# Kernel tuning notes

Measured on AMD Instinct MI355X. Metric: run time of the kernel, lower is better.

## Reference

```python
import jax, jax.numpy as jnp
import numpy as np

TOP_K = 2
CAPACITY_FACTOR = 1.25
EPSILON = 1e-06
AUX_LOSS_WEIGHT = 0.01
NUM_EXPERTS = 64


def setup_inputs() -> dict:
    key = jax.random.key(0)
    k1, k2 = jax.random.split(key, 2)
    x = jax.random.normal(k1, (32768, 1024), dtype=jnp.float32)
    w_gate = jax.random.normal(k2, (NUM_EXPERTS, 1024), dtype=jnp.float32) * 0.02
    b_gate = jnp.zeros((NUM_EXPERTS,), dtype=jnp.float32)
    return {"x": x, "w_gate": w_gate, "b_gate": b_gate}


def reference(x, w_gate, b_gate):
    # x: [N, dim]; w_gate: [E, dim]; b_gate: [E]
    n_tokens = x.shape[0]
    capacity = int(CAPACITY_FACTOR * n_tokens)  # static, like torch int(...)

    logits = jnp.einsum('nd,ed->ne', x, w_gate) + b_gate          # [N, E]
    raw_gate_scores = jax.nn.softmax(logits, axis=-1)             # [N, E]

    _, top_k_indices = jax.lax.top_k(raw_gate_scores, TOP_K)      # [N, k]
    rows = jnp.arange(n_tokens)[:, None]                          # [N, 1]
    mask = jnp.zeros_like(raw_gate_scores).at[rows, top_k_indices].set(1.0)

    masked_gate_scores = raw_gate_scores * mask                   # [N, E]
    denominators = masked_gate_scores.sum(axis=0, keepdims=True) + EPSILON
    gate_scores = masked_gate_scores / denominators * capacity    # [N, E]

    importance = raw_gate_scores.mean(axis=0)                     # [E]
    load = mask.mean(axis=0)                                      # [E]
    aux_loss = AUX_LOSS_WEIGHT * (importance * load).mean() * (NUM_EXPERTS ** 2)
    return gate_scores, aux_loss
```

## Files before the change

### kernel.cpp

```cpp
#include <hip/hip_runtime.h>
#include <cstdint>

typedef float f32x2 __attribute__((ext_vector_type(2)));
typedef float f32x4 __attribute__((ext_vector_type(4)));

constexpr int N_TOK = 32768;
constexpr int DIM   = 1024;
constexpr int NEXP  = 64;
constexpr float CAPACITY = 40960.0f;
constexpr float EPS_DEN  = 1e-6f;

__device__ float  g_sums[192];
__device__ float4 g_rec[N_TOK];

__global__ void init_sums() {
    if (threadIdx.x < 192) g_sums[threadIdx.x] = 0.0f;
}

__global__ __launch_bounds__(256, 2)
void gate_main(const float* __restrict__ x,
               const float* __restrict__ wg,
               const float* __restrict__ bg) {
    __shared__ float acT[NEXP * 4 * 64];
    __shared__ float ws[192];

    const int tid  = threadIdx.x;
    const int lane = tid & 63;
    const int q    = __builtin_amdgcn_readfirstlane(tid >> 6);
    const int row  = blockIdx.x * 64 + lane;

    if (tid < 192) ws[tid] = 0.0f;

    float acc[NEXP];
#pragma unroll
    for (int e = 0; e < NEXP; ++e) acc[e] = 0.0f;

    const float* xq = x  + (size_t)row * DIM + q * 256;
    const float* wq = wg + q * 256;

    f32x4 xa0, xa1, xa2, xa3;
    {
        const f32x4* xp = (const f32x4*)xq;
        xa0 = xp[0]; xa1 = xp[1]; xa2 = xp[2]; xa3 = xp[3];
    }

#pragma unroll 1
    for (int kc = 0; kc < 16; ++kc) {
        f32x4 xb0, xb1, xb2, xb3;
        if (kc + 1 < 16) {
            const f32x4* xp = (const f32x4*)(xq + (kc + 1) * 16);
            xb0 = xp[0]; xb1 = xp[1]; xb2 = xp[2]; xb3 = xp[3];
        }
#pragma unroll
        for (int e = 0; e < NEXP; ++e) {
            const f32x4* wp = (const f32x4*)(wq + e * DIM + kc * 16);
            f32x4 w0 = wp[0], w1 = wp[1], w2 = wp[2], w3 = wp[3];
            f32x2 t = {0.0f, 0.0f};
            t = __builtin_elementwise_fma((f32x2){xa0.x, xa0.y}, (f32x2){w0.x, w0.y}, t);
            t = __builtin_elementwise_fma((f32x2){xa0.z, xa0.w}, (f32x2){w0.z, w0.w}, t);
            t = __builtin_elementwise_fma((f32x2){xa1.x, xa1.y}, (f32x2){w1.x, w1.y}, t);
            t = __builtin_elementwise_fma((f32x2){xa1.z, xa1.w}, (f32x2){w1.z, w1.w}, t);
            t = __builtin_elementwise_fma((f32x2){xa2.x, xa2.y}, (f32x2){w2.x, w2.y}, t);
            t = __builtin_elementwise_fma((f32x2){xa2.z, xa2.w}, (f32x2){w2.z, w2.w}, t);
            t = __builtin_elementwise_fma((f32x2){xa3.x, xa3.y}, (f32x2){w3.x, w3.y}, t);
            t = __builtin_elementwise_fma((f32x2){xa3.z, xa3.w}, (f32x2){w3.z, w3.w}, t);
            acc[e] += t.x + t.y;
        }
        xa0 = xb0; xa1 = xb1; xa2 = xb2; xa3 = xb3;
    }

#pragma unroll
    for (int e = 0; e < NEXP; ++e)
        acT[(e * 4 + q) * 64 + lane] = acc[e];
    __syncthreads();

    if (q == 0) {
        float lg[NEXP];
#pragma unroll
        for (int e = 0; e < NEXP; ++e) {
            lg[e] = (acT[(e * 4 + 0) * 64 + lane] + acT[(e * 4 + 1) * 64 + lane])
                  + (acT[(e * 4 + 2) * 64 + lane] + acT[(e * 4 + 3) * 64 + lane]);
            lg[e] += bg[e];
        }

        float b1 = -INFINITY, b2 = -INFINITY; int i1 = 0, i2 = 0;
#pragma unroll
        for (int e = 0; e < NEXP; ++e) {
            float v = lg[e];
            if (v > b1)      { b2 = b1; i2 = i1; b1 = v; i1 = e; }
            else if (v > b2) { b2 = v;  i2 = e; }
        }

        float s = 0.0f;
#pragma unroll
        for (int e = 0; e < NEXP; ++e) {
            float t = expf(lg[e] - b1);
            lg[e] = t;
            s += t;
        }
        const float inv  = 1.0f / s;
        const float raw1 = inv;
        const float raw2 = expf(b2 - b1) * inv;

        float* rawT = acT;
#pragma unroll
        for (int e = 0; e < NEXP; ++e)
            rawT[lane * 65 + e] = lg[e] * inv;
        __asm__ volatile("" ::: "memory");
        float imp = 0.0f;
#pragma unroll
        for (int t = 0; t < 64; ++t)
            imp += rawT[t * 65 + lane];
        atomicAdd(&g_sums[64 + lane], imp);

        atomicAdd(&ws[i1], raw1);
        atomicAdd(&ws[i2], raw2);
        atomicAdd(&ws[128 + i1], 1.0f);
        atomicAdd(&ws[128 + i2], 1.0f);
        g_rec[row] = make_float4(raw1, raw2,
                                 __int_as_float(i1), __int_as_float(i2));
    }

    __syncthreads();
    if (tid < 64)                     atomicAdd(&g_sums[tid], ws[tid]);
    else if (tid >= 128 && tid < 192) atomicAdd(&g_sums[tid], ws[tid]);
}

__global__ __launch_bounds__(256)
void scatter_out(float* __restrict__ out) {
    __shared__ float scale_s[NEXP];
    int tid = threadIdx.x;
    if (tid < NEXP) {
        float den = g_sums[tid];
        scale_s[tid] = CAPACITY / (den + EPS_DEN);
        if (blockIdx.x == 0) {
            float prod = g_sums[64 + tid] * g_sums[128 + tid];
#pragma unroll
            for (int off = 32; off; off >>= 1) prod += __shfl_xor(prod, off);
            if (tid == 0) {
                out[(size_t)N_TOK * NEXP] =
                    0.64f * prod / ((float)N_TOK * (float)N_TOK);
            }
        }
    }
    __syncthreads();

    int row = blockIdx.x * 16 + (tid >> 4);
    int g   = tid & 15;

    float4 rec = g_rec[row];
    int i1 = __float_as_int(rec.z);
    int i2 = __float_as_int(rec.w);
    float s1 = rec.x * scale_s[i1];
    float s2 = rec.y * scale_s[i2];

    int base = g * 4;
    float4 o;
    o.x = (i1 == base + 0) ? s1 : ((i2 == base + 0) ? s2 : 0.0f);
    o.y = (i1 == base + 1) ? s1 : ((i2 == base + 1) ? s2 : 0.0f);
    o.z = (i1 == base + 2) ? s1 : ((i2 == base + 2) ? s2 : 0.0f);
    o.w = (i1 == base + 3) ? s1 : ((i2 == base + 3) ? s2 : 0.0f);

    ((float4*)out)[(size_t)row * 16 + g] = o;
}

extern "C" void kernel_launch(void* const* d_in, const int* in_sizes, int n_in,
                              void* d_out, int out_size, void* d_ws, size_t ws_size,
                              hipStream_t stream) {
    const float* x  = (const float*)d_in[0];
    const float* wg = (const float*)d_in[1];
    const float* bg = (const float*)d_in[2];
    float* out = (float*)d_out;

    hipLaunchKernelGGL(init_sums, dim3(1), dim3(256), 0, stream);
    hipLaunchKernelGGL(gate_main, dim3(N_TOK / 64), dim3(256), 0, stream,
                       x, wg, bg);
    hipLaunchKernelGGL(scatter_out, dim3(N_TOK / 16), dim3(256), 0, stream, out);
}
```

Before: 408.3 us.

## Split gating GEMM into register-tiled split-K kernel plus separate combine kernel

Replaces the per-row dot-product gate kernel with a split-K register-tiled GEMM. Each thread computes a 16-token by 4-expert tile, with weights staged through double-buffered, XOR-swizzled shared memory. Partial sums for the four K quarters go to a global buffer, and a new combine kernel does the bias, softmax, top-2 and statistics. This aims to remove the redundant per-thread weight loads and raise FMA reuse, at the cost of an extra 32 MB round trip for partials and one more launch.

Measured after the change: 578.0 us. +41.5%, slower.

```diff
diff --git a/kernel.cpp b/kernel.cpp
--- a/kernel.cpp
+++ b/kernel.cpp
@@ -1,7 +1,6 @@
 #include <hip/hip_runtime.h>
 #include <cstdint>
 
-typedef float f32x2 __attribute__((ext_vector_type(2)));
 typedef float f32x4 __attribute__((ext_vector_type(4)));
 
 constexpr int N_TOK = 32768;
@@ -12,118 +11,162 @@
 
 __device__ float  g_sums[192];
 __device__ float4 g_rec[N_TOK];
+__device__ float  g_part[4][NEXP][N_TOK];
 
 __global__ void init_sums() {
     if (threadIdx.x < 192) g_sums[threadIdx.x] = 0.0f;
 }
 
-__global__ __launch_bounds__(256, 2)
-void gate_main(const float* __restrict__ x,
-               const float* __restrict__ wg,
-               const float* __restrict__ bg) {
-    __shared__ float acT[NEXP * 4 * 64];
+#define MT 16
+#define NT 4
+
+__global__ __launch_bounds__(512, 2)
+void gemm_part(const float* __restrict__ x, const float* __restrict__ wg) {
+    __shared__ f32x4 wbuf[2][NEXP * 16];
+
+    const int tid  = threadIdx.x;
+    const int cc   = tid & 15;
+    const int rs   = tid >> 4;
+    const int kq   = blockIdx.x & 3;
+    const int tg   = blockIdx.x >> 2;
+    const int tbase = tg * 512 + rs * MT;
+
+    const float* xrow = x + (size_t)tbase * DIM + kq * 256;
+    const float* wq   = wg + kq * 256;
+
+    float acc[MT][NT];
+#pragma unroll
+    for (int m = 0; m < MT; ++m)
+#pragma unroll
+        for (int n = 0; n < NT; ++n) acc[m][n] = 0.0f;
+
+    f32x4 xa[MT], xb[MT], wst[2];
+
+#define PF(X, kk) do { _Pragma("unroll")                                      \
+    for (int m_ = 0; m_ < MT; ++m_)                                           \
+        X[m_] = *(const f32x4*)(xrow + (size_t)m_ * DIM + (kk) * 4);          \
+    } while (0)
+
+#define COMP(X, kk) do {                                                      \
+    const int k4s_ = (kk) & 15;                                               \
+    const int bf_  = ((kk) >> 4) & 1;                                         \
+    _Pragma("unroll")                                                         \
+    for (int n_ = 0; n_ < NT; ++n_) {                                         \
+        f32x4 w_ = wbuf[bf_][(4 * cc + n_) * 16 + (k4s_ ^ cc)];               \
+        _Pragma("unroll")                                                     \
+        for (int m_ = 0; m_ < MT; ++m_) {                                     \
+            acc[m_][n_] = fmaf(X[m_].x, w_.x, acc[m_][n_]);                   \
+            acc[m_][n_] = fmaf(X[m_].y, w_.y, acc[m_][n_]);                   \
+            acc[m_][n_] = fmaf(X[m_].z, w_.z, acc[m_][n_]);                   \
+            acc[m_][n_] = fmaf(X[m_].w, w_.w, acc[m_][n_]);                   \
+        }                                                                     \
+    } } while (0)
+
+#define WLOAD(c) do { _Pragma("unroll")                                       \
+    for (int i_ = 0; i_ < 2; ++i_) {                                          \
+        int j_ = tid + 512 * i_, e_ = j_ >> 4, ks_ = j_ & 15;                 \
+        wst[i_] = *(const f32x4*)(wq + (size_t)e_ * DIM + (c) * 64            \
+                                   + ((ks_ ^ ((e_ >> 2) & 15)) << 2));        \
+    } } while (0)
+
+#define WCOMMIT(c) do { _Pragma("unroll")                                     \
+    for (int i_ = 0; i_ < 2; ++i_)                                            \
+        wbuf[(c) & 1][tid + 512 * i_] = wst[i_];                              \
+    } while (0)
+
+    PF(xa, 0);
+    WLOAD(0);
+    WCOMMIT(0);
+    __syncthreads();
+
+    for (int kp = 0; kp < 32; ++kp) {
+        const int kk = kp * 2;
+        const int c  = kk >> 4;
+        if ((kk & 15) == 0 && c < 3) WLOAD(c + 1);
+        PF(xb, kk + 1);
+        COMP(xa, kk);
+        if (kp < 31) PF(xa, kk + 2);
+        COMP(xb, kk + 1);
+        if ((kk & 15) == 14 && c < 3) {
+            WCOMMIT(c + 1);
+            __syncthreads();
+        }
+    }
+
+#pragma unroll
+    for (int n = 0; n < NT; ++n) {
+        float* dst = &g_part[kq][4 * cc + n][tbase];
+#pragma unroll
+        for (int mg = 0; mg < 4; ++mg) {
+            f32x4 v = {acc[mg * 4 + 0][n], acc[mg * 4 + 1][n],
+                       acc[mg * 4 + 2][n], acc[mg * 4 + 3][n]};
+            *(f32x4*)(dst + mg * 4) = v;
+        }
+    }
+#undef PF
+#undef COMP
+#undef WLOAD
+#undef WCOMMIT
+}
+
+__global__ __launch_bounds__(128)
+void combine(const float* __restrict__ bg) {
+    __shared__ float rawT[128 * 65];
     __shared__ float ws[192];
 
-    const int tid  = threadIdx.x;
-    const int lane = tid & 63;
-    const int q    = __builtin_amdgcn_readfirstlane(tid >> 6);
-    const int row  = blockIdx.x * 64 + lane;
-
-    if (tid < 192) ws[tid] = 0.0f;
-
-    float acc[NEXP];
-#pragma unroll
-    for (int e = 0; e < NEXP; ++e) acc[e] = 0.0f;
-
-    const float* xq = x  + (size_t)row * DIM + q * 256;
-    const float* wq = wg + q * 256;
-
-    f32x4 xa0, xa1, xa2, xa3;
-    {
-        const f32x4* xp = (const f32x4*)xq;
-        xa0 = xp[0]; xa1 = xp[1]; xa2 = xp[2]; xa3 = xp[3];
-    }
-
-#pragma unroll 1
-    for (int kc = 0; kc < 16; ++kc) {
-        f32x4 xb0, xb1, xb2, xb3;
-        if (kc + 1 < 16) {
-            const f32x4* xp = (const f32x4*)(xq + (kc + 1) * 16);
-            xb0 = xp[0]; xb1 = xp[1]; xb2 = xp[2]; xb3 = xp[3];
-        }
-#pragma unroll
-        for (int e = 0; e < NEXP; ++e) {
-            const f32x4* wp = (const f32x4*)(wq + e * DIM + kc * 16);
-            f32x4 w0 = wp[0], w1 = wp[1], w2 = wp[2], w3 = wp[3];
-            f32x2 t = {0.0f, 0.0f};
-            t = __builtin_elementwise_fma((f32x2){xa0.x, xa0.y}, (f32x2){w0.x, w0.y}, t);
-            t = __builtin_elementwise_fma((f32x2){xa0.z, xa0.w}, (f32x2){w0.z, w0.w}, t);
-            t = __builtin_elementwise_fma((f32x2){xa1.x, xa1.y}, (f32x2){w1.x, w1.y}, t);
-            t = __builtin_elementwise_fma((f32x2){xa1.z, xa1.w}, (f32x2){w1.z, w1.w}, t);
-            t = __builtin_elementwise_fma((f32x2){xa2.x, xa2.y}, (f32x2){w2.x, w2.y}, t);
-            t = __builtin_elementwise_fma((f32x2){xa2.z, xa2.w}, (f32x2){w2.z, w2.w}, t);
-            t = __builtin_elementwise_fma((f32x2){xa3.x, xa3.y}, (f32x2){w3.x, w3.y}, t);
-            t = __builtin_elementwise_fma((f32x2){xa3.z, xa3.w}, (f32x2){w3.z, w3.w}, t);
-            acc[e] += t.x + t.y;
-        }
-        xa0 = xb0; xa1 = xb1; xa2 = xb2; xa3 = xb3;
-    }
-
-#pragma unroll
-    for (int e = 0; e < NEXP; ++e)
-        acT[(e * 4 + q) * 64 + lane] = acc[e];
-    __syncthreads();
-
-    if (q == 0) {
-        float lg[NEXP];
-#pragma unroll
-        for (int e = 0; e < NEXP; ++e) {
-            lg[e] = (acT[(e * 4 + 0) * 64 + lane] + acT[(e * 4 + 1) * 64 + lane])
-                  + (acT[(e * 4 + 2) * 64 + lane] + acT[(e * 4 + 3) * 64 + lane]);
-            lg[e] += bg[e];
-        }
-
-        float b1 = -INFINITY, b2 = -INFINITY; int i1 = 0, i2 = 0;
-#pragma unroll
-        for (int e = 0; e < NEXP; ++e) {
-            float v = lg[e];
-            if (v > b1)      { b2 = b1; i2 = i1; b1 = v; i1 = e; }
-            else if (v > b2) { b2 = v;  i2 = e; }
-        }
-
-        float s = 0.0f;
-#pragma unroll
-        for (int e = 0; e < NEXP; ++e) {
-            float t = expf(lg[e] - b1);
-            lg[e] = t;
-            s += t;
-        }
-        const float inv  = 1.0f / s;
-        const float raw1 = inv;
-        const float raw2 = expf(b2 - b1) * inv;
-
-        float* rawT = acT;
-#pragma unroll
-        for (int e = 0; e < NEXP; ++e)
-            rawT[lane * 65 + e] = lg[e] * inv;
-        __asm__ volatile("" ::: "memory");
+    const int tid = threadIdx.x;
+    const int t   = blockIdx.x * 128 + tid;
+
+    for (int i = tid; i < 192; i += 128) ws[i] = 0.0f;
+    __syncthreads();
+
+    float lg[NEXP];
+#pragma unroll
+    for (int e = 0; e < NEXP; ++e) {
+        lg[e] = (g_part[0][e][t] + g_part[1][e][t])
+              + (g_part[2][e][t] + g_part[3][e][t]) + bg[e];
+    }
+
+    float b1 = -INFINITY, b2 = -INFINITY; int i1 = 0, i2 = 0;
+#pragma unroll
+    for (int e = 0; e < NEXP; ++e) {
+        float v = lg[e];
+        if (v > b1)      { b2 = b1; i2 = i1; b1 = v; i1 = e; }
+        else if (v > b2) { b2 = v;  i2 = e; }
+    }
+
+    float s = 0.0f;
+#pragma unroll
+    for (int e = 0; e < NEXP; ++e) {
+        float ev = expf(lg[e] - b1);
+        lg[e] = ev;
+        s += ev;
+    }
+    const float inv  = 1.0f / s;
+    const float raw1 = inv;
+    const float raw2 = expf(b2 - b1) * inv;
+
+#pragma unroll
+    for (int e = 0; e < NEXP; ++e) rawT[tid * 65 + e] = lg[e] * inv;
+    __syncthreads();
+    if (tid < NEXP) {
         float imp = 0.0f;
 #pragma unroll
-        for (int t = 0; t < 64; ++t)
-            imp += rawT[t * 65 + lane];
-        atomicAdd(&g_sums[64 + lane], imp);
-
-        atomicAdd(&ws[i1], raw1);
-        atomicAdd(&ws[i2], raw2);
-        atomicAdd(&ws[128 + i1], 1.0f);
-        atomicAdd(&ws[128 + i2], 1.0f);
-        g_rec[row] = make_float4(raw1, raw2,
-                                 __int_as_float(i1), __int_as_float(i2));
-    }
-
-    __syncthreads();
-    if (tid < 64)                     atomicAdd(&g_sums[tid], ws[tid]);
-    else if (tid >= 128 && tid < 192) atomicAdd(&g_sums[tid], ws[tid]);
+        for (int tt = 0; tt < 128; ++tt) imp += rawT[tt * 65 + tid];
+        atomicAdd(&g_sums[64 + tid], imp);
+    }
+
+    atomicAdd(&ws[i1], raw1);
+    atomicAdd(&ws[i2], raw2);
+    atomicAdd(&ws[128 + i1], 1.0f);
+    atomicAdd(&ws[128 + i2], 1.0f);
+    g_rec[t] = make_float4(raw1, raw2, __int_as_float(i1), __int_as_float(i2));
+
+    __syncthreads();
+    if (tid < NEXP) {
+        atomicAdd(&g_sums[tid],       ws[tid]);
+        atomicAdd(&g_sums[128 + tid], ws[128 + tid]);
+    }
 }
 
 __global__ __launch_bounds__(256)
@@ -173,7 +216,7 @@
     float* out = (float*)d_out;
 
     hipLaunchKernelGGL(init_sums, dim3(1), dim3(256), 0, stream);
-    hipLaunchKernelGGL(gate_main, dim3(N_TOK / 64), dim3(256), 0, stream,
-                       x, wg, bg);
+    hipLaunchKernelGGL(gemm_part, dim3(256), dim3(512), 0, stream, x, wg);
+    hipLaunchKernelGGL(combine, dim3(N_TOK / 128), dim3(128), 0, stream, bg);
     hipLaunchKernelGGL(scatter_out, dim3(N_TOK / 16), dim3(256), 0, stream, out);
 }
```
